# Kernel optimization log

Measured on AMD Instinct MI355X. Metric: run time of the kernel, lower is better.

## Reference

```python
import jax, jax.numpy as jnp
import numpy as np

TAU = 0.1
EPS_NORM = 1e-12  # torch F.normalize clamp
EPS_DEN = 1e-6


def setup_inputs() -> dict:
    key = jax.random.key(0)
    k1, k2, k3, k4 = jax.random.split(key, 4)
    B, C, H, W = 4, 128, 64, 64
    feat_A = jax.random.normal(k1, (B, C, H, W), dtype=jnp.float32)
    feat_B = jax.random.normal(k2, (B, C, H, W), dtype=jnp.float32)
    H_mat = jax.random.normal(k3, (B, 3, 3), dtype=jnp.float32)
    valid_mask = jax.random.uniform(k4, (B, H, W), dtype=jnp.float32)
    return {"feat_A": feat_A, "feat_B": feat_B, "H_mat": H_mat, "valid_mask": valid_mask}


def _l2_normalize(x, axis):
    n = jnp.sqrt(jnp.sum(x * x, axis=axis, keepdims=True))
    return x / jnp.maximum(n, EPS_NORM)


def reference(feat_A, feat_B, H_mat, valid_mask):
    B, C, H, W = feat_A.shape
    HW = H * W
    fA = _l2_normalize(feat_A.reshape(B, C, HW), axis=1)  # [B, C, HW]
    fB = _l2_normalize(feat_B.reshape(B, C, HW), axis=1)  # [B, C, HW]
    # sim[b, n, m] = <fA[:, :, n], fB[:, :, m]> / tau
    sim = jnp.einsum('bcn,bcm->bnm', fA, fB) / TAU  # [B, HW, HW]
    # torch CE with input [B, HW, HW], labels arange(HW): class axis is 1,
    # so logits for position k are the column sim[b, :, k], target = k.
    lse = jax.nn.logsumexp(sim, axis=1)               # [B, HW] (over class axis)
    diag = jnp.einsum('bkk->bk', sim)                 # sim[b, k, k]
    loss = lse - diag                                  # [B, HW], per-position CE
    mask_flat = valid_mask.reshape(B, HW)
    return (loss * mask_flat).sum() / (mask_flat.sum() + EPS_DEN)
```

## Files before the change

### kernel.cpp

```cpp
#include <hip/hip_runtime.h>
#include <math.h>

#define BB 4
#define CC 128
#define HW 4096
#define SCF 3.798282565f

typedef short short8 __attribute__((ext_vector_type(8)));
typedef float f32x4 __attribute__((ext_vector_type(4)));

static __device__ inline unsigned short f2bf(float f) {
  unsigned int u = __float_as_uint(f);
  u += 0x7fffu + ((u >> 16) & 1u);
  return (unsigned short)(u >> 16);
}

__global__ __launch_bounds__(256) void k_prep(const float* __restrict__ fA,
                                              const float* __restrict__ fB,
                                              unsigned short* __restrict__ fAn,
                                              unsigned short* __restrict__ fBn,
                                              float* __restrict__ diag,
                                              float* __restrict__ expsum,
                                              float* __restrict__ acc) {
  __shared__ float sA[32 * 129];
  __shared__ float sB[32 * 129];
  __shared__ float red[3 * 256];

  const int bid = blockIdx.x;
  const int b   = bid >> 7;
  const int n0  = (bid & 127) * 32;
  const int tid = threadIdx.x;
  const int cR  = tid >> 5;
  const int n   = tid & 31;

  if (bid == 0 && tid == 0) { acc[0] = 0.f; acc[1] = 0.f; ((unsigned*)acc)[2] = 0u; }

  const float* pa = fA + (size_t)b * CC * HW + n0 + n;
  const float* pb = fB + (size_t)b * CC * HW + n0 + n;

  float ssa = 0.f, ssb = 0.f, dot = 0.f;
  #pragma unroll
  for (int it = 0; it < 16; ++it) {
    int c = it * 8 + cR;
    float va = pa[(size_t)c * HW];
    float vb = pb[(size_t)c * HW];
    sA[n * 129 + c] = va;
    sB[n * 129 + c] = vb;
    ssa = fmaf(va, va, ssa);
    ssb = fmaf(vb, vb, ssb);
    dot = fmaf(va, vb, dot);
  }
  red[tid] = ssa; red[256 + tid] = ssb; red[512 + tid] = dot;
  __syncthreads();

  if (tid < 32) {
    float sa = 0.f, sb = 0.f, dt = 0.f;
    #pragma unroll
    for (int k = 0; k < 8; ++k) {
      sa += red[k * 32 + tid];
      sb += red[256 + k * 32 + tid];
      dt += red[512 + k * 32 + tid];
    }
    float ia = 1.f / fmaxf(sqrtf(sa), 1e-12f);
    float ib = 1.f / fmaxf(sqrtf(sb), 1e-12f);
    int gidx = b * HW + n0 + tid;
    diag[gidx]   = dt * ia * ib * 10.f;
    expsum[gidx] = 0.f;
    red[tid]      = ia * SCF;
    red[32 + tid] = ib * SCF;
  }
  __syncthreads();

  #pragma unroll
  for (int r = 0; r < 2; ++r) {
    int L  = r * 256 + tid;
    int nn = L >> 4;
    int q  = L & 15;
    int c0 = (q ^ (nn & 7)) * 8;
    size_t base = ((size_t)b * HW + n0 + nn) * 128 + q * 8;
    {
      float sc = red[nn];
      const float* s = &sA[nn * 129 + c0];
      uint4 v;
      v.x = f2bf(s[0]*sc) | ((unsigned)f2bf(s[1]*sc) << 16);
      v.y = f2bf(s[2]*sc) | ((unsigned)f2bf(s[3]*sc) << 16);
      v.z = f2bf(s[4]*sc) | ((unsigned)f2bf(s[5]*sc) << 16);
      v.w = f2bf(s[6]*sc) | ((unsigned)f2bf(s[7]*sc) << 16);
      *(uint4*)(fAn + base) = v;
    }
    {
      float sc = red[32 + nn];
      const float* s = &sB[nn * 129 + c0];
      uint4 v;
      v.x = f2bf(s[0]*sc) | ((unsigned)f2bf(s[1]*sc) << 16);
      v.y = f2bf(s[2]*sc) | ((unsigned)f2bf(s[3]*sc) << 16);
      v.z = f2bf(s[4]*sc) | ((unsigned)f2bf(s[5]*sc) << 16);
      v.w = f2bf(s[6]*sc) | ((unsigned)f2bf(s[7]*sc) << 16);
      *(uint4*)(fBn + base) = v;
    }
  }
}

__global__ __launch_bounds__(256, 2) void k_main(const unsigned short* __restrict__ fAn,
                                                 const unsigned short* __restrict__ fBn,
                                                 float* __restrict__ expsum,
                                                 const float* __restrict__ diag,
                                                 const float* __restrict__ mask,
                                                 float* __restrict__ acc,
                                                 float* __restrict__ out) {
  __shared__ unsigned short lds[2 * 16384];
  unsigned short* buf0 = lds;
  unsigned short* buf1 = lds + 16384;
  __shared__ bool lastFlag;

  const int bid = blockIdx.x;
  const int x   = bid & 7;
  const int t   = bid >> 3;
  const int b   = x & 3;
  const int nq  = (x >> 2) | ((t & 1) << 1);
  const int mt  = t >> 1;
  const int m0  = mt * 128;
  const int nbase = nq * 1024;
  const int tid = threadIdx.x;

  const int wv   = tid >> 6;
  const int lane = tid & 63;
  const int ml   = lane & 15;
  const int g    = lane >> 4;
  const int wn   = (wv & 1) * 64;
  const int wm   = (wv >> 1) * 64;

  auto stage = [&](const unsigned short* gsrc, unsigned short* dst) {
    #pragma unroll
    for (int r = 0; r < 8; ++r) {
      int L = r * 256 + tid;
      __builtin_amdgcn_global_load_lds(
          (const __attribute__((address_space(1))) unsigned int*)(gsrc + (size_t)L * 8),
          (__attribute__((address_space(3))) unsigned int*)(dst + L * 8), 16, 0, 0);
    }
  };
  const unsigned short* gAbase = fAn + ((size_t)b * HW + nbase) * 128;

  stage(fBn + ((size_t)b * HW + m0) * 128, buf1);
  stage(gAbase, buf0);
  __syncthreads();

  short8 bf[4][4], af[4][4];
  #pragma unroll
  for (int kc = 0; kc < 4; ++kc) {
    int q = kc * 4 + g;
    #pragma unroll
    for (int j = 0; j < 4; ++j) {
      int nb = wm + j * 16 + ml;
      bf[kc][j] = *(const short8*)(buf1 + nb * 128 + ((q ^ (nb & 7)) * 8));
    }
    #pragma unroll
    for (int i = 0; i < 4; ++i) {
      int na = wn + i * 16 + ml;
      af[kc][i] = *(const short8*)(buf0 + na * 128 + ((q ^ (na & 7)) * 8));
    }
  }
  __syncthreads();
  stage(gAbase + (size_t)1 * 16384, buf1);

  float colAcc[4] = {0.f, 0.f, 0.f, 0.f};

  for (int it = 0; it < 8; ++it) {
    f32x4 acc4[4][4] = {};
    #pragma unroll
    for (int kc = 0; kc < 4; ++kc)
      #pragma unroll
      for (int i = 0; i < 4; ++i)
        #pragma unroll
        for (int j = 0; j < 4; ++j)
          acc4[i][j] = __builtin_amdgcn_mfma_f32_16x16x32_bf16(af[kc][i], bf[kc][j], acc4[i][j], 0, 0, 0);
    #pragma unroll
    for (int j = 0; j < 4; ++j) {
      float e = 0.f;
      #pragma unroll
      for (int i = 0; i < 4; ++i)
        #pragma unroll
        for (int r = 0; r < 4; ++r)
          e += exp2f(acc4[i][j][r]);
      colAcc[j] += e;
    }
    if (it == 7) break;
    __syncthreads();
    const unsigned short* bufc = (it & 1) ? buf0 : buf1;
    #pragma unroll
    for (int kc = 0; kc < 4; ++kc) {
      int q = kc * 4 + g;
      #pragma unroll
      for (int i = 0; i < 4; ++i) {
        int na = wn + i * 16 + ml;
        af[kc][i] = *(const short8*)(bufc + na * 128 + ((q ^ (na & 7)) * 8));
      }
    }
    if (it < 6)
      stage(gAbase + (size_t)(it + 2) * 16384, (it & 1) ? buf1 : buf0);
  }

  #pragma unroll
  for (int j = 0; j < 4; ++j) {
    float e = colAcc[j];
    e += __shfl_xor(e, 16, 64);
    e += __shfl_xor(e, 32, 64);
    if (lane < 16)
      atomicAdd(&expsum[(size_t)b * HW + m0 + wm + j * 16 + lane], e);
  }

  __syncthreads();
  if (tid == 0) {
    __threadfence();
    lastFlag = (atomicAdd((unsigned*)(acc + 2), 1u) == 511u);
  }
  __syncthreads();
  if (lastFlag) {
    float num = 0.f, den = 0.f;
    #pragma unroll 4
    for (int i = tid; i < BB * HW; i += 256) {
      float es = __hip_atomic_load(expsum + i, __ATOMIC_RELAXED, __HIP_MEMORY_SCOPE_AGENT);
      float mv = mask[i];
      num = fmaf(mv, __logf(es) - diag[i], num);
      den += mv;
    }
    #pragma unroll
    for (int off = 32; off; off >>= 1) {
      num += __shfl_down(num, off, 64);
      den += __shfl_down(den, off, 64);
    }
    float* red = (float*)lds;
    if (lane == 0) { red[wv] = num; red[8 + wv] = den; }
    __syncthreads();
    if (tid == 0) {
      float n = red[0] + red[1] + red[2] + red[3];
      float d = red[8] + red[9] + red[10] + red[11];
      out[0] = n / (d + 1e-6f);
    }
  }
}

extern "C" void kernel_launch(void* const* d_in, const int* in_sizes, int n_in,
                              void* d_out, int out_size, void* d_ws, size_t ws_size,
                              hipStream_t stream) {
  const float* feat_A = (const float*)d_in[0];
  const float* feat_B = (const float*)d_in[1];
  const float* vmask  = (const float*)d_in[3];

  unsigned short* fAn = (unsigned short*)d_ws;
  unsigned short* fBn = fAn + (size_t)BB * HW * CC;
  float* diag   = (float*)(fBn + (size_t)BB * HW * CC);
  float* expsum = diag + BB * HW;
  float* acc    = expsum + BB * HW;
  float* out    = (float*)d_out;

  k_prep<<<512, 256, 0, stream>>>(feat_A, feat_B, fAn, fBn, diag, expsum, acc);
  k_main<<<512, 256, 0, stream>>>(fAn, fBn, expsum, diag, vmask, acc, out);
}
```

Measured before the change: 113.0 us.

## Halve A tile per iteration and read A fragments from LDS each step

Each iteration of the main loop now covers 64 A rows in double-buffered LDS, down from 128, so the loop runs 16 times instead of 8. A fragments are loaded from LDS inside the k-loop rather than held in registers across iterations. The prefetch of the next tile is issued at the start of each iteration, and there is one barrier per step. This lowers register pressure and LDS footprint, which may help occupancy, but it adds more barriers and per-step LDS reads.

```diff
diff --git a/kernel.cpp b/kernel.cpp
--- a/kernel.cpp
+++ b/kernel.cpp
@@ -108,10 +108,8 @@
                                                  const float* __restrict__ mask,
                                                  float* __restrict__ acc,
                                                  float* __restrict__ out) {
-  __shared__ unsigned short lds[2 * 16384];
-  unsigned short* buf0 = lds;
-  unsigned short* buf1 = lds + 16384;
-  __shared__ bool lastFlag;
+  __shared__ unsigned short sB[16384];
+  __shared__ unsigned short sA[2][8192];
 
   const int bid = blockIdx.x;
   const int x   = bid & 7;
@@ -127,77 +125,86 @@
   const int lane = tid & 63;
   const int ml   = lane & 15;
   const int g    = lane >> 4;
-  const int wn   = (wv & 1) * 64;
+  const int wn   = (wv & 1) * 32;
   const int wm   = (wv >> 1) * 64;
 
-  auto stage = [&](const unsigned short* gsrc, unsigned short* dst) {
+  const unsigned short* gAbase = fAn + ((size_t)b * HW + nbase) * 128;
+
+  {
+    const unsigned short* gB = fBn + ((size_t)b * HW + m0) * 128;
     #pragma unroll
     for (int r = 0; r < 8; ++r) {
       int L = r * 256 + tid;
       __builtin_amdgcn_global_load_lds(
-          (const __attribute__((address_space(1))) unsigned int*)(gsrc + (size_t)L * 8),
-          (__attribute__((address_space(3))) unsigned int*)(dst + L * 8), 16, 0, 0);
-    }
-  };
-  const unsigned short* gAbase = fAn + ((size_t)b * HW + nbase) * 128;
-
-  stage(fBn + ((size_t)b * HW + m0) * 128, buf1);
-  stage(gAbase, buf0);
-  __syncthreads();
-
-  short8 bf[4][4], af[4][4];
+          (const __attribute__((address_space(1))) unsigned int*)(gB + (size_t)L * 8),
+          (__attribute__((address_space(3))) unsigned int*)(sB + L * 8), 16, 0, 0);
+    }
+    #pragma unroll
+    for (int r = 0; r < 4; ++r) {
+      int L = r * 256 + tid;
+      __builtin_amdgcn_global_load_lds(
+          (const __attribute__((address_space(1))) unsigned int*)(gAbase + (size_t)L * 8),
+          (__attribute__((address_space(3))) unsigned int*)(sA[0] + L * 8), 16, 0, 0);
+    }
+  }
+  __syncthreads();
+
+  short8 bf[4][4];
   #pragma unroll
   for (int kc = 0; kc < 4; ++kc) {
     int q = kc * 4 + g;
     #pragma unroll
     for (int j = 0; j < 4; ++j) {
       int nb = wm + j * 16 + ml;
-      bf[kc][j] = *(const short8*)(buf1 + nb * 128 + ((q ^ (nb & 7)) * 8));
-    }
-    #pragma unroll
-    for (int i = 0; i < 4; ++i) {
-      int na = wn + i * 16 + ml;
-      af[kc][i] = *(const short8*)(buf0 + na * 128 + ((q ^ (na & 7)) * 8));
-    }
-  }
-  __syncthreads();
-  stage(gAbase + (size_t)1 * 16384, buf1);
+      bf[kc][j] = *(const short8*)(sB + nb * 128 + ((q ^ (nb & 7)) * 8));
+    }
+  }
 
   float colAcc[4] = {0.f, 0.f, 0.f, 0.f};
 
-  for (int it = 0; it < 8; ++it) {
-    f32x4 acc4[4][4] = {};
-    #pragma unroll
-    for (int kc = 0; kc < 4; ++kc)
+  for (int it = 0; it < 16; ++it) {
+    if (it < 15) {
+      const unsigned short* gA = gAbase + (size_t)(it + 1) * 8192;
+      unsigned short* dst = sA[(it + 1) & 1];
       #pragma unroll
-      for (int i = 0; i < 4; ++i)
-        #pragma unroll
-        for (int j = 0; j < 4; ++j)
-          acc4[i][j] = __builtin_amdgcn_mfma_f32_16x16x32_bf16(af[kc][i], bf[kc][j], acc4[i][j], 0, 0, 0);
+      for (int r = 0; r < 4; ++r) {
+        int L = r * 256 + tid;
+        __builtin_amdgcn_global_load_lds(
+            (const __attribute__((address_space(1))) unsigned int*)(gA + (size_t)L * 8),
+            (__attribute__((address_space(3))) unsigned int*)(dst + L * 8), 16, 0, 0);
+      }
+    }
+
+    const unsigned short* bufc = sA[it & 1];
+    f32x4 acc4[2][4] = {};
+    #pragma unroll
+    for (int kc = 0; kc < 4; ++kc) {
+      int q = kc * 4 + g;
+      short8 af0, af1;
+      {
+        int na = wn + ml;
+        af0 = *(const short8*)(bufc + na * 128 + ((q ^ (na & 7)) * 8));
+        na = wn + 16 + ml;
+        af1 = *(const short8*)(bufc + na * 128 + ((q ^ (na & 7)) * 8));
+      }
+      #pragma unroll
+      for (int j = 0; j < 4; ++j) {
+        acc4[0][j] = __builtin_amdgcn_mfma_f32_16x16x32_bf16(af0, bf[kc][j], acc4[0][j], 0, 0, 0);
+        acc4[1][j] = __builtin_amdgcn_mfma_f32_16x16x32_bf16(af1, bf[kc][j], acc4[1][j], 0, 0, 0);
+      }
+    }
     #pragma unroll
     for (int j = 0; j < 4; ++j) {
       float e = 0.f;
       #pragma unroll
-      for (int i = 0; i < 4; ++i)
+      for (int i = 0; i < 2; ++i)
         #pragma unroll
         for (int r = 0; r < 4; ++r)
           e += exp2f(acc4[i][j][r]);
       colAcc[j] += e;
     }
-    if (it == 7) break;
+
     __syncthreads();
-    const unsigned short* bufc = (it & 1) ? buf0 : buf1;
-    #pragma unroll
-    for (int kc = 0; kc < 4; ++kc) {
-      int q = kc * 4 + g;
-      #pragma unroll
-      for (int i = 0; i < 4; ++i) {
-        int na = wn + i * 16 + ml;
-        af[kc][i] = *(const short8*)(bufc + na * 128 + ((q ^ (na & 7)) * 8));
-      }
-    }
-    if (it < 6)
-      stage(gAbase + (size_t)(it + 2) * 16384, (it & 1) ? buf1 : buf0);
   }
 
   #pragma unroll
@@ -209,13 +216,14 @@
       atomicAdd(&expsum[(size_t)b * HW + m0 + wm + j * 16 + lane], e);
   }
 
+  unsigned* flag = (unsigned*)sA;
   __syncthreads();
   if (tid == 0) {
     __threadfence();
-    lastFlag = (atomicAdd((unsigned*)(acc + 2), 1u) == 511u);
-  }
-  __syncthreads();
-  if (lastFlag) {
+    flag[0] = (atomicAdd((unsigned*)(acc + 2), 1u) == 511u) ? 1u : 0u;
+  }
+  __syncthreads();
+  if (flag[0]) {
     float num = 0.f, den = 0.f;
     #pragma unroll 4
     for (int i = tid; i < BB * HW; i += 256) {
@@ -229,7 +237,7 @@
       num += __shfl_down(num, off, 64);
       den += __shfl_down(den, off, 64);
     }
-    float* red = (float*)lds;
+    float* red = (float*)sB;
     if (lane == 0) { red[wv] = num; red[8 + wv] = den; }
     __syncthreads();
     if (tid == 0) {
```

Result: slower. 115.8 us (+2.5%).
